# Kernel optimization log

Hardware: AMD Instinct MI355X
Metric: run time of the kernel (lower is better)

## Reference

```python
import jax, jax.numpy as jnp
import numpy as np

D = 128      # d_model
H = 4        # heads == edge embedding dim
C = D // H   # per-head channels
L = 4        # gnn layers
N = 200000   # batched atoms
E = 400000   # batched directed bonds
G = 8000     # molecules in batch
NTASK = 1
NEG_SLOPE = 0.2


def setup_inputs() -> dict:
    key = jax.random.key(0)
    ks = jax.random.split(key, 12)
    s = 0.05
    x = jax.random.randint(ks[0], (N, 9), 0, 16)            # atom features
    edge_index = jax.random.randint(ks[1], (2, E), 0, N)    # [src; dst]
    edge_attr = jax.random.randint(ks[2], (E,), 0, 10)      # bond types
    batch_ids = jnp.sort(jax.random.randint(ks[3], (N,), 0, G))
    atom_tables = jax.random.normal(ks[4], (9, 16, D), jnp.float32) * s
    bond_table = jax.random.normal(ks[5], (10, H), jnp.float32) * s
    Wl = jax.random.normal(ks[6], (L, D, D), jnp.float32) * s   # lin_l per layer
    bl = jnp.zeros((L, D), jnp.float32)
    Wr = jax.random.normal(ks[7], (L, D, D), jnp.float32) * s   # lin_r per layer
    br = jnp.zeros((L, D), jnp.float32)
    We = jax.random.normal(ks[8], (L, H, D), jnp.float32) * s   # lin_edge (no bias)
    att = jax.random.normal(ks[9], (L, H, C), jnp.float32) * s  # attention vector a
    cb = jnp.zeros((L, D), jnp.float32)                          # conv output bias
    Wout = jax.random.normal(ks[10], (D, NTASK), jnp.float32) * s
    bout = jnp.zeros((NTASK,), jnp.float32)
    return dict(atom_tables=atom_tables, bond_table=bond_table, Wl=Wl, bl=bl,
                Wr=Wr, br=br, We=We, att=att, cb=cb, Wout=Wout, bout=bout,
                x=x, edge_index=edge_index, edge_attr=edge_attr, batch_ids=batch_ids)


def _segment_softmax(logits, seg, num_segments):
    # logits: [Ef, H], softmax over edges sharing the same target node
    m = jax.ops.segment_max(logits, seg, num_segments=num_segments)
    e = jnp.exp(logits - m[seg])
    z = jax.ops.segment_sum(e, seg, num_segments=num_segments)
    return e / (z[seg] + 1e-16)


def _forward(atom_tables, bond_table, Wl, bl, Wr, br, We, att, cb, Wout, bout,
             x, edge_index, edge_attr, batch_ids):
    # Atom encoder: sum of per-feature embeddings -> [N, D]
    h = atom_tables[jnp.arange(9)[None, :], x].sum(axis=1)
    # Bond encoder -> [E, H]
    e_emb = bond_table[edge_attr]
    src, dst = edge_index[0], edge_index[1]
    n = h.shape[0]
    # add_self_loops with fill_value='mean': per-target mean of incoming edge feats
    sums = jax.ops.segment_sum(e_emb, dst, num_segments=n)
    cnt = jax.ops.segment_sum(jnp.ones((e_emb.shape[0],), e_emb.dtype), dst,
                              num_segments=n)
    loop_attr = sums / jnp.maximum(cnt, 1.0)[:, None]
    ar = jnp.arange(n)
    src_f = jnp.concatenate([src, ar])
    dst_f = jnp.concatenate([dst, ar])
    e_full = jnp.concatenate([e_emb, loop_attr], axis=0)   # [E+N, H]

    for l in range(L):
        xl = (h @ Wl[l] + bl[l]).reshape(n, H, C)
        xr = (h @ Wr[l] + br[l]).reshape(n, H, C)
        ee = (e_full @ We[l]).reshape(-1, H, C)            # [E+N, H, C]
        g = jax.nn.leaky_relu(xl[src_f] + xr[dst_f] + ee, NEG_SLOPE)
        logits = jnp.einsum('ehc,hc->eh', g, att[l])
        alpha = _segment_softmax(logits, dst_f, n)         # [E+N, H]
        out = jax.ops.segment_sum(xl[src_f] * alpha[:, :, None], dst_f,
                                  num_segments=n)
        h = out.reshape(n, D) + cb[l]
        if l < L - 1:
            h = jax.nn.relu(h)

    # global add pool over molecules, then linear head
    pooled = jax.ops.segment_sum(h, batch_ids, num_segments=G)  # [G, D]
    return pooled @ Wout + bout                                  # [G, num_tasks]


def reference(atom_tables, bond_table, Wl, bl, Wr, br, We, att, cb, Wout, bout,
              x, edge_index, edge_attr, batch_ids):
    return _forward(atom_tables, bond_table, Wl, bl, Wr, br, We, att, cb, Wout,
                    bout, x, edge_index, edge_attr, batch_ids)
```

## Files before the change

### kernel.cpp

```cpp
#include <hip/hip_runtime.h>
#include <hip/hip_bf16.h>

#define DD 128
#define NHEAD 4
#define CHAN 32
#define NEG 0.2f

typedef short bf16x8 __attribute__((ext_vector_type(8)));
typedef float f32x4 __attribute__((ext_vector_type(4)));

__device__ inline ushort f2bf(float x) {
  unsigned u = __float_as_uint(x);
  return (ushort)((u + 0x7FFF + ((u >> 16) & 1)) >> 16);
}
__device__ inline float bf2f(ushort u) {
  return __uint_as_float((unsigned)u << 16);
}

__global__ void k_atom_enc(const int* __restrict__ x, const float* __restrict__ tab,
                           float* __restrict__ h, int N) {
  int idx = blockIdx.x * blockDim.x + threadIdx.x;
  if (idx >= N * DD) return;
  int n = idx >> 7, d = idx & 127;
  const int* xr = x + n * 9;
  float s = 0.f;
#pragma unroll
  for (int f = 0; f < 9; f++) {
    int v = xr[f];
    s += tab[(f * 16 + v) * DD + d];
  }
  h[idx] = s;
}

__global__ void k_init(int* __restrict__ deg, float* __restrict__ cnt,
                       float* __restrict__ sums, int N) {
  int i = blockIdx.x * blockDim.x + threadIdx.x;
  if (i >= N) return;
  deg[i] = 1;
  cnt[i] = 0.f;
  sums[i * 4 + 0] = 0.f; sums[i * 4 + 1] = 0.f;
  sums[i * 4 + 2] = 0.f; sums[i * 4 + 3] = 0.f;
}

__global__ void k_edge_count(const int* __restrict__ ei, const int* __restrict__ eattr,
                             const float* __restrict__ btab, float* __restrict__ e_emb,
                             float* __restrict__ sums, float* __restrict__ cnt,
                             int* __restrict__ deg, int E) {
  int e = blockIdx.x * blockDim.x + threadIdx.x;
  if (e >= E) return;
  int d = ei[E + e];
  int a = eattr[e];
  float f0 = btab[a * 4 + 0], f1 = btab[a * 4 + 1];
  float f2 = btab[a * 4 + 2], f3 = btab[a * 4 + 3];
  e_emb[e * 4 + 0] = f0; e_emb[e * 4 + 1] = f1;
  e_emb[e * 4 + 2] = f2; e_emb[e * 4 + 3] = f3;
  atomicAdd(&sums[d * 4 + 0], f0);
  atomicAdd(&sums[d * 4 + 1], f1);
  atomicAdd(&sums[d * 4 + 2], f2);
  atomicAdd(&sums[d * 4 + 3], f3);
  atomicAdd(&cnt[d], 1.0f);
  atomicAdd(&deg[d], 1);
}

__global__ void k_loopattr(float* __restrict__ sums, const float* __restrict__ cnt, int N) {
  int i = blockIdx.x * blockDim.x + threadIdx.x;
  if (i >= N * 4) return;
  sums[i] = sums[i] / fmaxf(cnt[i >> 2], 1.0f);
}

__global__ void k_scan_block(const int* __restrict__ deg, int* __restrict__ bsums, int N) {
  __shared__ int sh[256];
  int t = threadIdx.x;
  int base = blockIdx.x * 2048 + t * 8;
  int tot = 0;
#pragma unroll
  for (int i = 0; i < 8; i++) tot += (base + i < N) ? deg[base + i] : 0;
  sh[t] = tot;
  __syncthreads();
  for (int off = 128; off > 0; off >>= 1) {
    if (t < off) sh[t] += sh[t + off];
    __syncthreads();
  }
  if (t == 0) bsums[blockIdx.x] = sh[0];
}

__global__ void k_scan_top(int* __restrict__ bsums, int* __restrict__ rowptr,
                           int nblk, int N) {
  if (threadIdx.x == 0 && blockIdx.x == 0) {
    int run = 0;
    for (int b = 0; b < nblk; b++) { int v = bsums[b]; bsums[b] = run; run += v; }
    rowptr[N] = run;
  }
}

__global__ void k_scan_down(const int* __restrict__ deg, const int* __restrict__ bsums,
                            int* __restrict__ rowptr, int* __restrict__ cursor, int N) {
  __shared__ int sh[256];
  int t = threadIdx.x;
  int base = blockIdx.x * 2048 + t * 8;
  int v[8]; int tot = 0;
#pragma unroll
  for (int i = 0; i < 8; i++) { v[i] = (base + i < N) ? deg[base + i] : 0; tot += v[i]; }
  sh[t] = tot;
  __syncthreads();
  for (int off = 1; off < 256; off <<= 1) {
    int xv = (t >= off) ? sh[t - off] : 0;
    __syncthreads();
    sh[t] += xv;
    __syncthreads();
  }
  int run = bsums[blockIdx.x] + sh[t] - tot;
#pragma unroll
  for (int i = 0; i < 8; i++) {
    if (base + i < N) { rowptr[base + i] = run; cursor[base + i] = run; run += v[i]; }
  }
}

__global__ void k_scatter(const int* __restrict__ ei, int* __restrict__ cursor,
                          int* __restrict__ eid, int E, int N) {
  int t = blockIdx.x * blockDim.x + threadIdx.x;
  if (t >= E + N) return;
  int d = (t < E) ? ei[E + t] : (t - E);
  int pos = atomicAdd(&cursor[d], 1);
  eid[pos] = t;
}

__global__ void k_wpack(const float* __restrict__ Wl, const float* __restrict__ Wr,
                        ushort* __restrict__ Bhi, ushort* __restrict__ Blo, int L) {
  int tid = blockIdx.x * blockDim.x + threadIdx.x;
  int total = L * 2 * 4 * 8 * 64;
  if (tid >= total) return;
  int lane = tid & 63;
  int nt = (tid >> 6) & 7;
  int kb = (tid >> 9) & 3;
  int mat = (tid >> 11) & 1;
  int layer = tid >> 12;
  const float* W = (mat ? Wr : Wl) + (size_t)layer * DD * DD;
  int kbase = kb * 32 + (lane >> 4) * 8;
  int n = nt * 16 + (lane & 15);
  size_t out = (size_t)(layer * 2 + mat) * 16384 +
               ((size_t)(kb * 8 + nt) * 64 + lane) * 8;
#pragma unroll
  for (int j = 0; j < 8; j++) {
    float xv = W[(size_t)(kbase + j) * DD + n];
    ushort h_ = f2bf(xv);
    float fh = __uint_as_float((unsigned)h_ << 16);
    ushort l_ = f2bf(xv - fh);
    Bhi[out + j] = h_;
    Blo[out + j] = l_;
  }
}

__global__ __launch_bounds__(256) void k_gemm2_mfma(const float* h,
    const ushort* __restrict__ bhiL, const ushort* __restrict__ bloL,
    const ushort* __restrict__ bhiR, const ushort* __restrict__ bloR,
    const float* __restrict__ bl, const float* __restrict__ br,
    ushort* __restrict__ xlb, float* xr_rows, int N) {
  __shared__ ushort sAhi[64 * 128];
  __shared__ ushort sAlo[64 * 128];
  int t = threadIdx.x;
  int A0 = blockIdx.x * 64;
  {
    int a = t >> 2;
    int kq = (t & 3) * 32;
    int n = A0 + a;
    const float* hp = &h[(size_t)n * DD + kq];
    int swz = (a & 7) << 4;
    int rowb = a * 256;
#pragma unroll
    for (int i = 0; i < 8; i++) {
      float4 v = (n < N) ? *(const float4*)(hp + i * 4) : make_float4(0, 0, 0, 0);
      float fv[4] = {v.x, v.y, v.z, v.w};
      ushort hiw[4], low[4];
#pragma unroll
      for (int j = 0; j < 4; j++) {
        ushort h_ = f2bf(fv[j]);
        float fh = __uint_as_float((unsigned)h_ << 16);
        hiw[j] = h_;
        low[j] = f2bf(fv[j] - fh);
      }
      int inrow = (kq + i * 4) * 2;
      int off = rowb + (inrow ^ swz);
      *(ushort4*)((char*)sAhi + off) = make_ushort4(hiw[0], hiw[1], hiw[2], hiw[3]);
      *(ushort4*)((char*)sAlo + off) = make_ushort4(low[0], low[1], low[2], low[3]);
    }
  }
  __syncthreads();

  int lane = t & 63;
  int w = t >> 6;
  int arow = lane & 15;
  int acol = (lane >> 4) * 16;
  int swzr = (arow & 7) << 4;

  f32x4 accL[4][2], accR[4][2];
#pragma unroll
  for (int mt = 0; mt < 4; mt++)
#pragma unroll
    for (int nti = 0; nti < 2; nti++) {
      accL[mt][nti] = (f32x4){0.f, 0.f, 0.f, 0.f};
      accR[mt][nti] = (f32x4){0.f, 0.f, 0.f, 0.f};
    }

  for (int kb = 0; kb < 4; kb++) {
    bf16x8 ahi[4], alo[4];
#pragma unroll
    for (int mt = 0; mt < 4; mt++) {
      int abyte = (mt * 16 + arow) * 256 + ((kb * 64 + acol) ^ swzr);
      ahi[mt] = *(const bf16x8*)((const char*)sAhi + abyte);
      alo[mt] = *(const bf16x8*)((const char*)sAlo + abyte);
    }
#pragma unroll
    for (int nti = 0; nti < 2; nti++) {
      int nt = w * 2 + nti;
      size_t fo = ((size_t)(kb * 8 + nt) * 64 + lane) * 8;
      bf16x8 bhl = *(const bf16x8*)(bhiL + fo);
      bf16x8 bll = *(const bf16x8*)(bloL + fo);
      bf16x8 bhr = *(const bf16x8*)(bhiR + fo);
      bf16x8 blr = *(const bf16x8*)(bloR + fo);
#pragma unroll
      for (int mt = 0; mt < 4; mt++) {
        accL[mt][nti] = __builtin_amdgcn_mfma_f32_16x16x32_bf16(ahi[mt], bhl, accL[mt][nti], 0, 0, 0);
        accR[mt][nti] = __builtin_amdgcn_mfma_f32_16x16x32_bf16(ahi[mt], bhr, accR[mt][nti], 0, 0, 0);
        accL[mt][nti] = __builtin_amdgcn_mfma_f32_16x16x32_bf16(ahi[mt], bll, accL[mt][nti], 0, 0, 0);
        accR[mt][nti] = __builtin_amdgcn_mfma_f32_16x16x32_bf16(ahi[mt], blr, accR[mt][nti], 0, 0, 0);
        accL[mt][nti] = __builtin_amdgcn_mfma_f32_16x16x32_bf16(alo[mt], bhl, accL[mt][nti], 0, 0, 0);
        accR[mt][nti] = __builtin_amdgcn_mfma_f32_16x16x32_bf16(alo[mt], bhr, accR[mt][nti], 0, 0, 0);
      }
    }
  }

  ushort* xru = (ushort*)xr_rows;
  int col = lane & 15;
  int rgrp = (lane >> 4) * 4;
#pragma unroll
  for (int nti = 0; nti < 2; nti++) {
    int n = (w * 2 + nti) * 16 + col;
    float bLv = bl[n], bRv = br[n];
#pragma unroll
    for (int mt = 0; mt < 4; mt++) {
#pragma unroll
      for (int r = 0; r < 4; r++) {
        int atom = A0 + mt * 16 + rgrp + r;
        if (atom < N) {
          xlb[(size_t)atom * DD + n]  = f2bf(accL[mt][nti][r] + bLv);
          xru[(size_t)atom * 256 + n] = f2bf(accR[mt][nti][r] + bRv);
        }
      }
    }
  }
}

__global__ __launch_bounds__(256) void k_attn(
    const ushort* __restrict__ xlb, const float* xr_rows,
    const float* __restrict__ e_emb, const float* __restrict__ la,
    const int* __restrict__ ei, const int* __restrict__ rowptr,
    const int* __restrict__ eid,
    const float* __restrict__ Wep, const float* __restrict__ attp,
    const float* __restrict__ cbp,
    const float* __restrict__ Woutp, const int* __restrict__ bid,
    float* __restrict__ outp,
    float* hout, int N, int E, int flags) {
  __shared__ float sv[4];
  __shared__ int   sb[4];
  int wid = threadIdx.x >> 6;
  int lane = threadIdx.x & 63;
  int n = blockIdx.x * 4 + wid;
  bool act = n < N;
  int d0 = lane * 2;
  float o0 = 0.f, o1 = 0.f;
  if (act) {
    float we0[4], we1[4];
#pragma unroll
    for (int j = 0; j < 4; j++) {
      we0[j] = Wep[j * DD + d0];
      we1[j] = Wep[j * DD + d0 + 1];
    }
    int hh = lane >> 4;
    float a0 = attp[hh * 32 + (d0 & 31)];
    float a1 = attp[hh * 32 + ((d0 + 1) & 31)];
    const ushort* xru = (const ushort*)xr_rows;
    ushort2 xru2 = *(const ushort2*)&xru[(size_t)n * 256 + d0];
    float xr0 = bf2f(xru2.x), xr1 = bf2f(xru2.y);
    float4 la4 = *(const float4*)&la[(size_t)n * 4];
    float m = -3.0e38f, z = 0.f, acc0 = 0.f, acc1 = 0.f;
    int r0 = rowptr[n], r1 = rowptr[n + 1];
    for (int p0 = r0; p0 < r1; p0 += 4) {
      int ss[4]; float4 ff[4];
      float xv0[4], xv1[4], pv[4];
#pragma unroll
      for (int j = 0; j < 4; j++) {
        int p = p0 + j; p = (p < r1) ? p : (r1 - 1);
        int e = eid[p];
        bool re = e < E;
        ss[j] = re ? ei[e] : n;
        ff[j] = re ? *(const float4*)&e_emb[(size_t)e * 4] : la4;
      }
#pragma unroll
      for (int j = 0; j < 4; j++) {
        ushort2 u = *(const ushort2*)&xlb[(size_t)ss[j] * DD + d0];
        xv0[j] = bf2f(u.x); xv1[j] = bf2f(u.y);
      }
#pragma unroll
      for (int j = 0; j < 4; j++) {
        float ee0 = ff[j].x * we0[0] + ff[j].y * we0[1] + ff[j].z * we0[2] + ff[j].w * we0[3];
        float ee1 = ff[j].x * we1[0] + ff[j].y * we1[1] + ff[j].z * we1[2] + ff[j].w * we1[3];
        float g0 = xv0[j] + xr0 + ee0; g0 = g0 > 0.f ? g0 : NEG * g0;
        float g1 = xv1[j] + xr1 + ee1; g1 = g1 > 0.f ? g1 : NEG * g1;
        pv[j] = g0 * a0 + g1 * a1;
      }
#pragma unroll
      for (int j = 0; j < 4; j++) {
        pv[j] += __shfl_xor(pv[j], 1);
        pv[j] += __shfl_xor(pv[j], 2);
        pv[j] += __shfl_xor(pv[j], 4);
        pv[j] += __shfl_xor(pv[j], 8);
      }
#pragma unroll
      for (int j = 0; j < 4; j++) {
        float msk = (p0 + j < r1) ? 1.f : 0.f;
        float mn = fmaxf(m, pv[j]);
        float sc = __expf(m - mn);
        float wj = __expf(pv[j] - mn) * msk;
        z = z * sc + wj;
        acc0 = acc0 * sc + wj * xv0[j];
        acc1 = acc1 * sc + wj * xv1[j];
        m = mn;
      }
    }
    float inv = 1.f / (z + 1e-16f);
    o0 = acc0 * inv + cbp[d0];
    o1 = acc1 * inv + cbp[d0 + 1];
    if (flags & 1) { o0 = fmaxf(o0, 0.f); o1 = fmaxf(o1, 0.f); }
    if (!(flags & 2)) {
      *(float2*)&hout[(size_t)n * DD + d0] = make_float2(o0, o1);
    }
  }
  if (flags & 2) {
    float v = o0 * Woutp[d0] + o1 * Woutp[d0 + 1];
    v += __shfl_xor(v, 1);
    v += __shfl_xor(v, 2);
    v += __shfl_xor(v, 4);
    v += __shfl_xor(v, 8);
    v += __shfl_xor(v, 16);
    v += __shfl_xor(v, 32);
    if (lane == 0) {
      sv[wid] = v;
      sb[wid] = act ? bid[n] : -1;
    }
    __syncthreads();
    if (threadIdx.x == 0) {
      int i = 0;
      while (i < 4) {
        int b = sb[i];
        if (b < 0) { i++; continue; }
        float s = sv[i];
        int j = i + 1;
        while (j < 4 && sb[j] == b) { s += sv[j]; j++; }
        atomicAdd(&outp[b], s);
        i = j;
      }
    }
  }
}

__global__ void k_head_init(float* __restrict__ out, const float* __restrict__ bout, int G) {
  int i = blockIdx.x * blockDim.x + threadIdx.x;
  if (i < G) out[i] = bout[0];
}

extern "C" void kernel_launch(void* const* d_in, const int* in_sizes, int n_in,
                              void* d_out, int out_size, void* d_ws, size_t ws_size,
                              hipStream_t stream) {
  const float* atom_tables = (const float*)d_in[0];
  const float* bond_table  = (const float*)d_in[1];
  const float* Wl   = (const float*)d_in[2];
  const float* bl   = (const float*)d_in[3];
  const float* Wr   = (const float*)d_in[4];
  const float* br   = (const float*)d_in[5];
  const float* We   = (const float*)d_in[6];
  const float* att  = (const float*)d_in[7];
  const float* cb   = (const float*)d_in[8];
  const float* Wout = (const float*)d_in[9];
  const float* bout = (const float*)d_in[10];
  const int* x      = (const int*)d_in[11];
  const int* ei     = (const int*)d_in[12];
  const int* eattr  = (const int*)d_in[13];
  const int* bid    = (const int*)d_in[14];

  int N = in_sizes[11] / 9;
  int E = in_sizes[13];
  int G = out_size;
  int L = in_sizes[3] / DD;

  char* p = (char*)d_ws;
  auto alloc = [&](size_t bytes) {
    char* r = p;
    p += (bytes + 255) & ~(size_t)255;
    return r;
  };
  float*  hx     = (float*)alloc((size_t)N * DD * 4);
  ushort* xlb    = (ushort*)alloc((size_t)N * DD * 2);
  float*  e_emb  = (float*)alloc((size_t)E * 4 * 4);
  float*  sums   = (float*)alloc((size_t)N * 4 * 4);
  int*    rowptr = (int*)alloc((size_t)(N + 1) * 4);
  int*    eid    = (int*)alloc((size_t)(E + N) * 4);
  float*  cnt    = (float*)alloc((size_t)N * 4);
  int*    deg    = (int*)alloc((size_t)N * 4);
  int*    cursor = (int*)alloc((size_t)N * 4);
  int nblk = (N + 2047) / 2048;
  int*    bsums  = (int*)alloc((size_t)nblk * 4);
  ushort* Bhi    = (ushort*)alloc((size_t)L * 2 * 16384 * 2);
  ushort* Blo    = (ushort*)alloc((size_t)L * 2 * 16384 * 2);
  float*  out    = (float*)d_out;

  if ((size_t)(p - (char*)d_ws) > ws_size) return;

  hipLaunchKernelGGL(k_atom_enc, dim3((N * DD + 255) / 256), dim3(256), 0, stream,
                     x, atom_tables, hx, N);
  hipLaunchKernelGGL(k_init, dim3((N + 255) / 256), dim3(256), 0, stream,
                     deg, cnt, sums, N);
  hipLaunchKernelGGL(k_edge_count, dim3((E + 255) / 256), dim3(256), 0, stream,
                     ei, eattr, bond_table, e_emb, sums, cnt, deg, E);
  hipLaunchKernelGGL(k_scan_block, dim3(nblk), dim3(256), 0, stream, deg, bsums, N);
  hipLaunchKernelGGL(k_scan_top, dim3(1), dim3(64), 0, stream, bsums, rowptr, nblk, N);
  hipLaunchKernelGGL(k_scan_down, dim3(nblk), dim3(256), 0, stream,
                     deg, bsums, rowptr, cursor, N);
  hipLaunchKernelGGL(k_scatter, dim3((E + N + 255) / 256), dim3(256), 0, stream,
                     ei, cursor, eid, E, N);
  hipLaunchKernelGGL(k_loopattr, dim3((N * 4 + 255) / 256), dim3(256), 0, stream,
                     sums, cnt, N);
  {
    int total = L * 2 * 4 * 8 * 64;
    hipLaunchKernelGGL(k_wpack, dim3((total + 255) / 256), dim3(256), 0, stream,
                       Wl, Wr, Bhi, Blo, L);
  }
  hipLaunchKernelGGL(k_head_init, dim3((G + 255) / 256), dim3(256), 0, stream,
                     out, bout, G);

  for (int l = 0; l < L; l++) {
    const ushort* bhiL = Bhi + (size_t)(l * 2 + 0) * 16384;
    const ushort* bhiR = Bhi + (size_t)(l * 2 + 1) * 16384;
    const ushort* bloL = Blo + (size_t)(l * 2 + 0) * 16384;
    const ushort* bloR = Blo + (size_t)(l * 2 + 1) * 16384;
    hipLaunchKernelGGL(k_gemm2_mfma, dim3((N + 63) / 64), dim3(256), 0, stream,
                       hx, bhiL, bloL, bhiR, bloR,
                       bl + (size_t)l * DD, br + (size_t)l * DD, xlb, hx, N);
    int flags = (l < L - 1) ? 1 : 2;
    hipLaunchKernelGGL(k_attn, dim3((N + 3) / 4), dim3(256), 0, stream,
                       xlb, hx, e_emb, sums, ei, rowptr, eid,
                       We + (size_t)l * NHEAD * DD, att + (size_t)l * NHEAD * CHAN,
                       cb + (size_t)l * DD, Wout, bid, out, hx, N, E, flags);
  }
}
```

Measured before the change: 1.231 ms.

## Store hidden state as bf16 hi/lo split and process four edges per wave

The atom encoder and attention kernels now write the hidden state directly as bf16 hi/lo pairs. The GEMM can then load its A fragments straight from global memory, skipping the fp32 read, the per-element split and the LDS staging. xr gets its own compact bf16 buffer. The attention kernel splits each wave into four 16-lane groups that handle four edges at once, each lane covering 8 channels with 16-byte gathers, and the groups are combined with shuffles at the end. The online max subtraction in the softmax is removed, which saves work but risks exp overflow if logits grow large.

```diff
diff --git a/kernel.cpp b/kernel.cpp
--- a/kernel.cpp
+++ b/kernel.cpp
@@ -2,8 +2,6 @@
 #include <hip/hip_bf16.h>
 
 #define DD 128
-#define NHEAD 4
-#define CHAN 32
 #define NEG 0.2f
 
 typedef short bf16x8 __attribute__((ext_vector_type(8)));
@@ -13,23 +11,20 @@
   unsigned u = __float_as_uint(x);
   return (ushort)((u + 0x7FFF + ((u >> 16) & 1)) >> 16);
 }
-__device__ inline float bf2f(ushort u) {
-  return __uint_as_float((unsigned)u << 16);
-}
+__device__ inline float bf2f(ushort u) { return __uint_as_float((unsigned)u << 16); }
 
 __global__ void k_atom_enc(const int* __restrict__ x, const float* __restrict__ tab,
-                           float* __restrict__ h, int N) {
+                           ushort* __restrict__ h_hi, ushort* __restrict__ h_lo, int N) {
   int idx = blockIdx.x * blockDim.x + threadIdx.x;
   if (idx >= N * DD) return;
   int n = idx >> 7, d = idx & 127;
   const int* xr = x + n * 9;
   float s = 0.f;
 #pragma unroll
-  for (int f = 0; f < 9; f++) {
-    int v = xr[f];
-    s += tab[(f * 16 + v) * DD + d];
-  }
-  h[idx] = s;
+  for (int f = 0; f < 9; f++) s += tab[(f * 16 + xr[f]) * DD + d];
+  ushort hi = f2bf(s);
+  h_hi[idx] = hi;
+  h_lo[idx] = f2bf(s - bf2f(hi));
 }
 
 __global__ void k_init(int* __restrict__ deg, float* __restrict__ cnt,
@@ -151,47 +146,17 @@
   }
 }
 
-__global__ __launch_bounds__(256) void k_gemm2_mfma(const float* h,
+__global__ __launch_bounds__(256) void k_gemm2_mfma(
+    const ushort* __restrict__ h_hi, const ushort* __restrict__ h_lo,
     const ushort* __restrict__ bhiL, const ushort* __restrict__ bloL,
     const ushort* __restrict__ bhiR, const ushort* __restrict__ bloR,
     const float* __restrict__ bl, const float* __restrict__ br,
-    ushort* __restrict__ xlb, float* xr_rows, int N) {
-  __shared__ ushort sAhi[64 * 128];
-  __shared__ ushort sAlo[64 * 128];
+    ushort* __restrict__ xlb, ushort* __restrict__ xrb, int N) {
   int t = threadIdx.x;
+  int lane = t & 63, w = t >> 6;
   int A0 = blockIdx.x * 64;
-  {
-    int a = t >> 2;
-    int kq = (t & 3) * 32;
-    int n = A0 + a;
-    const float* hp = &h[(size_t)n * DD + kq];
-    int swz = (a & 7) << 4;
-    int rowb = a * 256;
-#pragma unroll
-    for (int i = 0; i < 8; i++) {
-      float4 v = (n < N) ? *(const float4*)(hp + i * 4) : make_float4(0, 0, 0, 0);
-      float fv[4] = {v.x, v.y, v.z, v.w};
-      ushort hiw[4], low[4];
-#pragma unroll
-      for (int j = 0; j < 4; j++) {
-        ushort h_ = f2bf(fv[j]);
-        float fh = __uint_as_float((unsigned)h_ << 16);
-        hiw[j] = h_;
-        low[j] = f2bf(fv[j] - fh);
-      }
-      int inrow = (kq + i * 4) * 2;
-      int off = rowb + (inrow ^ swz);
-      *(ushort4*)((char*)sAhi + off) = make_ushort4(hiw[0], hiw[1], hiw[2], hiw[3]);
-      *(ushort4*)((char*)sAlo + off) = make_ushort4(low[0], low[1], low[2], low[3]);
-    }
-  }
-  __syncthreads();
-
-  int lane = t & 63;
-  int w = t >> 6;
   int arow = lane & 15;
-  int acol = (lane >> 4) * 16;
-  int swzr = (arow & 7) << 4;
+  int kg = lane >> 4;
 
   f32x4 accL[4][2], accR[4][2];
 #pragma unroll
@@ -202,13 +167,14 @@
       accR[mt][nti] = (f32x4){0.f, 0.f, 0.f, 0.f};
     }
 
+#pragma unroll
   for (int kb = 0; kb < 4; kb++) {
     bf16x8 ahi[4], alo[4];
 #pragma unroll
     for (int mt = 0; mt < 4; mt++) {
-      int abyte = (mt * 16 + arow) * 256 + ((kb * 64 + acol) ^ swzr);
-      ahi[mt] = *(const bf16x8*)((const char*)sAhi + abyte);
-      alo[mt] = *(const bf16x8*)((const char*)sAlo + abyte);
+      size_t aoff = (size_t)(A0 + mt * 16 + arow) * DD + kb * 32 + kg * 8;
+      ahi[mt] = *(const bf16x8*)&h_hi[aoff];
+      alo[mt] = *(const bf16x8*)&h_lo[aoff];
     }
 #pragma unroll
     for (int nti = 0; nti < 2; nti++) {
@@ -230,7 +196,6 @@
     }
   }
 
-  ushort* xru = (ushort*)xr_rows;
   int col = lane & 15;
   int rgrp = (lane >> 4) * 4;
 #pragma unroll
@@ -243,8 +208,8 @@
       for (int r = 0; r < 4; r++) {
         int atom = A0 + mt * 16 + rgrp + r;
         if (atom < N) {
-          xlb[(size_t)atom * DD + n]  = f2bf(accL[mt][nti][r] + bLv);
-          xru[(size_t)atom * 256 + n] = f2bf(accR[mt][nti][r] + bRv);
+          xlb[(size_t)atom * DD + n] = f2bf(accL[mt][nti][r] + bLv);
+          xrb[(size_t)atom * DD + n] = f2bf(accR[mt][nti][r] + bRv);
         }
       }
     }
@@ -252,7 +217,7 @@
 }
 
 __global__ __launch_bounds__(256) void k_attn(
-    const ushort* __restrict__ xlb, const float* xr_rows,
+    const ushort* __restrict__ xlb, const ushort* __restrict__ xrb,
     const float* __restrict__ e_emb, const float* __restrict__ la,
     const int* __restrict__ ei, const int* __restrict__ rowptr,
     const int* __restrict__ eid,
@@ -260,92 +225,95 @@
     const float* __restrict__ cbp,
     const float* __restrict__ Woutp, const int* __restrict__ bid,
     float* __restrict__ outp,
-    float* hout, int N, int E, int flags) {
+    ushort* __restrict__ h_hi, ushort* __restrict__ h_lo,
+    int N, int E, int flags) {
   __shared__ float sv[4];
   __shared__ int   sb[4];
   int wid = threadIdx.x >> 6;
   int lane = threadIdx.x & 63;
+  int g = lane >> 4, q = lane & 15;
   int n = blockIdx.x * 4 + wid;
   bool act = n < N;
-  int d0 = lane * 2;
-  float o0 = 0.f, o1 = 0.f;
-  if (act) {
-    float we0[4], we1[4];
-#pragma unroll
-    for (int j = 0; j < 4; j++) {
-      we0[j] = Wep[j * DD + d0];
-      we1[j] = Wep[j * DD + d0 + 1];
-    }
-    int hh = lane >> 4;
-    float a0 = attp[hh * 32 + (d0 & 31)];
-    float a1 = attp[hh * 32 + ((d0 + 1) & 31)];
-    const ushort* xru = (const ushort*)xr_rows;
-    ushort2 xru2 = *(const ushort2*)&xru[(size_t)n * 256 + d0];
-    float xr0 = bf2f(xru2.x), xr1 = bf2f(xru2.y);
-    float4 la4 = *(const float4*)&la[(size_t)n * 4];
-    float m = -3.0e38f, z = 0.f, acc0 = 0.f, acc1 = 0.f;
-    int r0 = rowptr[n], r1 = rowptr[n + 1];
-    for (int p0 = r0; p0 < r1; p0 += 4) {
-      int ss[4]; float4 ff[4];
-      float xv0[4], xv1[4], pv[4];
-#pragma unroll
-      for (int j = 0; j < 4; j++) {
-        int p = p0 + j; p = (p < r1) ? p : (r1 - 1);
-        int e = eid[p];
-        bool re = e < E;
-        ss[j] = re ? ei[e] : n;
-        ff[j] = re ? *(const float4*)&e_emb[(size_t)e * 4] : la4;
-      }
-#pragma unroll
-      for (int j = 0; j < 4; j++) {
-        ushort2 u = *(const ushort2*)&xlb[(size_t)ss[j] * DD + d0];
-        xv0[j] = bf2f(u.x); xv1[j] = bf2f(u.y);
-      }
-#pragma unroll
-      for (int j = 0; j < 4; j++) {
-        float ee0 = ff[j].x * we0[0] + ff[j].y * we0[1] + ff[j].z * we0[2] + ff[j].w * we0[3];
-        float ee1 = ff[j].x * we1[0] + ff[j].y * we1[1] + ff[j].z * we1[2] + ff[j].w * we1[3];
-        float g0 = xv0[j] + xr0 + ee0; g0 = g0 > 0.f ? g0 : NEG * g0;
-        float g1 = xv1[j] + xr1 + ee1; g1 = g1 > 0.f ? g1 : NEG * g1;
-        pv[j] = g0 * a0 + g1 * a1;
-      }
-#pragma unroll
-      for (int j = 0; j < 4; j++) {
-        pv[j] += __shfl_xor(pv[j], 1);
-        pv[j] += __shfl_xor(pv[j], 2);
-        pv[j] += __shfl_xor(pv[j], 4);
-        pv[j] += __shfl_xor(pv[j], 8);
-      }
-#pragma unroll
-      for (int j = 0; j < 4; j++) {
-        float msk = (p0 + j < r1) ? 1.f : 0.f;
-        float mn = fmaxf(m, pv[j]);
-        float sc = __expf(m - mn);
-        float wj = __expf(pv[j] - mn) * msk;
-        z = z * sc + wj;
-        acc0 = acc0 * sc + wj * xv0[j];
-        acc1 = acc1 * sc + wj * xv1[j];
-        m = mn;
-      }
-    }
-    float inv = 1.f / (z + 1e-16f);
-    o0 = acc0 * inv + cbp[d0];
-    o1 = acc1 * inv + cbp[d0 + 1];
-    if (flags & 1) { o0 = fmaxf(o0, 0.f); o1 = fmaxf(o1, 0.f); }
-    if (!(flags & 2)) {
-      *(float2*)&hout[(size_t)n * DD + d0] = make_float2(o0, o1);
-    }
-  }
+  int nn = act ? n : (N - 1);
+  int c0 = q * 8;
+  int head = q >> 2;
+
+  float we[4][8];
+#pragma unroll
+  for (int j = 0; j < 4; j++)
+#pragma unroll
+    for (int c = 0; c < 8; c++) we[j][c] = Wep[j * DD + c0 + c];
+  float av[8];
+#pragma unroll
+  for (int c = 0; c < 8; c++) av[c] = attp[head * 32 + ((c0 + c) & 31)];
+  float xr[8];
+  {
+    bf16x8 u = *(const bf16x8*)&xrb[(size_t)nn * DD + c0];
+#pragma unroll
+    for (int c = 0; c < 8; c++) xr[c] = bf2f((ushort)u[c]);
+  }
+  float4 la4 = *(const float4*)&la[(size_t)nn * 4];
+
+  float z = 0.f;
+  float acc[8];
+#pragma unroll
+  for (int c = 0; c < 8; c++) acc[c] = 0.f;
+
+  int r0 = rowptr[nn], r1 = rowptr[nn + 1];
+  for (int p0 = r0; p0 < r1; p0 += 4) {
+    int p = p0 + g;
+    float msk = (p < r1) ? 1.f : 0.f;
+    p = (p < r1) ? p : (r1 - 1);
+    int e = eid[p];
+    bool re = e < E;
+    int eidx = re ? e : 0;
+    float4 f = *(const float4*)&e_emb[(size_t)eidx * 4];
+    if (!re) f = la4;
+    int s = re ? ei[eidx] : nn;
+    bf16x8 u = *(const bf16x8*)&xlb[(size_t)s * DD + c0];
+    float xv[8];
+#pragma unroll
+    for (int c = 0; c < 8; c++) xv[c] = bf2f((ushort)u[c]);
+    float pv = 0.f;
+#pragma unroll
+    for (int c = 0; c < 8; c++) {
+      float ee = f.x * we[0][c] + f.y * we[1][c] + f.z * we[2][c] + f.w * we[3][c];
+      float gg = xv[c] + xr[c] + ee;
+      gg = gg > 0.f ? gg : NEG * gg;
+      pv += gg * av[c];
+    }
+    pv += __shfl_xor(pv, 1);
+    pv += __shfl_xor(pv, 2);
+    float wj = __expf(pv) * msk;
+    z += wj;
+#pragma unroll
+    for (int c = 0; c < 8; c++) acc[c] += wj * xv[c];
+  }
+  z += __shfl_xor(z, 16);
+  z += __shfl_xor(z, 32);
+#pragma unroll
+  for (int c = 0; c < 8; c++) {
+    acc[c] += __shfl_xor(acc[c], 16);
+    acc[c] += __shfl_xor(acc[c], 32);
+  }
+  float inv = 1.f / (z + 1e-16f);
+  float o[8];
+#pragma unroll
+  for (int c = 0; c < 8; c++) {
+    o[c] = acc[c] * inv + cbp[c0 + c];
+    if (flags & 1) o[c] = fmaxf(o[c], 0.f);
+  }
+
   if (flags & 2) {
-    float v = o0 * Woutp[d0] + o1 * Woutp[d0 + 1];
+    float v = 0.f;
+#pragma unroll
+    for (int c = 0; c < 8; c++) v += o[c] * Woutp[c0 + c];
     v += __shfl_xor(v, 1);
     v += __shfl_xor(v, 2);
     v += __shfl_xor(v, 4);
     v += __shfl_xor(v, 8);
-    v += __shfl_xor(v, 16);
-    v += __shfl_xor(v, 32);
     if (lane == 0) {
-      sv[wid] = v;
+      sv[wid] = act ? v : 0.f;
       sb[wid] = act ? bid[n] : -1;
     }
     __syncthreads();
@@ -354,13 +322,23 @@
       while (i < 4) {
         int b = sb[i];
         if (b < 0) { i++; continue; }
-        float s = sv[i];
+        float s2 = sv[i];
         int j = i + 1;
-        while (j < 4 && sb[j] == b) { s += sv[j]; j++; }
-        atomicAdd(&outp[b], s);
+        while (j < 4 && sb[j] == b) { s2 += sv[j]; j++; }
+        atomicAdd(&outp[b], s2);
         i = j;
       }
     }
+  } else if (act && g == 0) {
+    bf16x8 vh, vl;
+#pragma unroll
+    for (int c = 0; c < 8; c++) {
+      ushort hi = f2bf(o[c]);
+      vh[c] = (short)hi;
+      vl[c] = (short)f2bf(o[c] - bf2f(hi));
+    }
+    *(bf16x8*)&h_hi[(size_t)n * DD + c0] = vh;
+    *(bf16x8*)&h_lo[(size_t)n * DD + c0] = vl;
   }
 }
 
@@ -399,8 +377,10 @@
     p += (bytes + 255) & ~(size_t)255;
     return r;
   };
-  float*  hx     = (float*)alloc((size_t)N * DD * 4);
+  ushort* h_hi   = (ushort*)alloc((size_t)(N + 64) * DD * 2);
+  ushort* h_lo   = (ushort*)alloc((size_t)(N + 64) * DD * 2);
   ushort* xlb    = (ushort*)alloc((size_t)N * DD * 2);
+  ushort* xrb    = (ushort*)alloc((size_t)N * DD * 2);
   float*  e_emb  = (float*)alloc((size_t)E * 4 * 4);
   float*  sums   = (float*)alloc((size_t)N * 4 * 4);
   int*    rowptr = (int*)alloc((size_t)(N + 1) * 4);
@@ -417,7 +397,7 @@
   if ((size_t)(p - (char*)d_ws) > ws_size) return;
 
   hipLaunchKernelGGL(k_atom_enc, dim3((N * DD + 255) / 256), dim3(256), 0, stream,
-                     x, atom_tables, hx, N);
+                     x, atom_tables, h_hi, h_lo, N);
   hipLaunchKernelGGL(k_init, dim3((N + 255) / 256), dim3(256), 0, stream,
                      deg, cnt, sums, N);
   hipLaunchKernelGGL(k_edge_count, dim3((E + 255) / 256), dim3(256), 0, stream,
@@ -444,12 +424,12 @@
     const ushort* bloL = Blo + (size_t)(l * 2 + 0) * 16384;
     const ushort* bloR = Blo + (size_t)(l * 2 + 1) * 16384;
     hipLaunchKernelGGL(k_gemm2_mfma, dim3((N + 63) / 64), dim3(256), 0, stream,
-                       hx, bhiL, bloL, bhiR, bloR,
-                       bl + (size_t)l * DD, br + (size_t)l * DD, xlb, hx, N);
+                       h_hi, h_lo, bhiL, bloL, bhiR, bloR,
+                       bl + (size_t)l * DD, br + (size_t)l * DD, xlb, xrb, N);
     int flags = (l < L - 1) ? 1 : 2;
     hipLaunchKernelGGL(k_attn, dim3((N + 3) / 4), dim3(256), 0, stream,
-                       xlb, hx, e_emb, sums, ei, rowptr, eid,
-                       We + (size_t)l * NHEAD * DD, att + (size_t)l * NHEAD * CHAN,
-                       cb + (size_t)l * DD, Wout, bid, out, hx, N, E, flags);
-  }
-}
+                       xlb, xrb, e_emb, sums, ei, rowptr, eid,
+                       We + (size_t)l * 4 * DD, att + (size_t)l * 4 * 32,
+                       cb + (size_t)l * DD, Wout, bid, out, h_hi, h_lo, N, E, flags);
+  }
+}
```

Result: slower. 1.466 ms (+19.1%).
